# Optimization experiments

Measured on AMD Instinct MI355X. Metric: run time of the kernel, lower is better.

Reference implementation:

```python
import jax, jax.numpy as jnp
import numpy as np

B, L, V = 64, 512, 32000
E, H, D = 64, 512, 1024   # embed dim, LSTM hidden, bidirectional dim
NH, KD = 8, 64            # attention heads, key_dim
TOPK = 5
BN_EPS = 1e-3             # keras BatchNormalization default epsilon


def _run_lstm(x, Wx, Wh, b):
    """Keras-style LSTM (gate order i,f,g,o). x: [B,T,Din]. Returns (seq [B,T,H], last [B,H])."""
    Bn, Hn = x.shape[0], Wh.shape[0]
    z = jnp.einsum('btd,dk->btk', x, Wx) + b  # precompute input contribution [B,T,4H]
    def step(carry, zt):
        h, c = carry
        g = zt + h @ Wh
        i, f, gg, o = jnp.split(g, 4, axis=-1)
        c = jax.nn.sigmoid(f) * c + jax.nn.sigmoid(i) * jnp.tanh(gg)
        h = jax.nn.sigmoid(o) * jnp.tanh(c)
        return (h, c), h
    init = (jnp.zeros((Bn, Hn), x.dtype), jnp.zeros((Bn, Hn), x.dtype))
    (hT, _), hs = jax.lax.scan(step, init, jnp.swapaxes(z, 0, 1))
    return jnp.swapaxes(hs, 0, 1), hT


def _bilstm_seq(x, fWx, fWh, fb, bWx, bWh, bb):
    hf, _ = _run_lstm(x, fWx, fWh, fb)
    hb, _ = _run_lstm(x[:, ::-1], bWx, bWh, bb)
    return jnp.concatenate([hf, hb[:, ::-1]], axis=-1)


def _bilstm_last(x, fWx, fWh, fb, bWx, bWh, bb):
    _, hf = _run_lstm(x, fWx, fWh, fb)
    _, hb = _run_lstm(x[:, ::-1], bWx, bWh, bb)
    return jnp.concatenate([hf, hb], axis=-1)


def _cos(x):
    return x / (jnp.linalg.norm(x, axis=-1, keepdims=True) + 1e-6)


def _topk_gather(q, keys, values, k, weight=None):
    """Cosine-similarity top-k retrieval: q [B,64], keys/values [N,64] -> [B,k,64]."""
    sim = _cos(q) @ _cos(keys).T          # [B,N]
    if weight is not None:
        sim = sim * weight                # importance / confidence weighting
    _, idx = jax.lax.top_k(sim, k)
    return values[idx]                    # gather -> [B,k,64]


def _forward(tokens, emb,
             l1f_Wx, l1f_Wh, l1f_b, l1b_Wx, l1b_Wh, l1b_b,
             l2f_Wx, l2f_Wh, l2f_b, l2b_Wx, l2b_Wh, l2b_b,
             Wq, bq, Wk, bk, Wv, bv, Wo, bo,
             mq_W, mq_b,
             ext_keys, ext_vals, form_emb, conc_keys, conc_vals,
             st_mem, lt_mem, lt_imp, inf_mem, inf_conf,
             rs_W, rs_b, bn_gamma, bn_beta, bn_mean, bn_var,
             out_W, out_b, fin_W, fin_b):
    # _process_input
    x = emb[tokens]                                                   # [B,L,64]
    x = _bilstm_seq(x, l1f_Wx, l1f_Wh, l1f_b, l1b_Wx, l1b_Wh, l1b_b)  # [B,L,1024]
    x = _bilstm_last(x, l2f_Wx, l2f_Wh, l2f_b, l2b_Wx, l2b_Wh, l2b_b) # [B,1024]
    # _apply_attention: MHA over a length-1 sequence
    xs = x[:, None, :]                                                # [B,1,1024]
    q = jnp.einsum('bse,ehd->bshd', xs, Wq) + bq
    k = jnp.einsum('bse,ehd->bshd', xs, Wk) + bk
    v = jnp.einsum('bse,ehd->bshd', xs, Wv) + bv
    att = jax.nn.softmax(jnp.einsum('bshd,bthd->bhst', q, k) / jnp.sqrt(jnp.float32(KD)), axis=-1)
    ctx = jnp.einsum('bhst,bthd->bshd', att, v)
    x = (jnp.einsum('bshd,hde->bse', ctx, Wo) + bo)[:, 0]             # [B,1024]
    # _query_memories: six-bank gather/combine
    query = x @ mq_W + mq_b                                           # [B,64]
    m_ext = jax.nn.softmax(query @ ext_keys.T, axis=-1) @ ext_vals    # [B,64]
    m_form = _topk_gather(query, form_emb, form_emb, TOPK)            # [B,5,64]
    m_conc = _topk_gather(query, conc_keys, conc_vals, TOPK)          # [B,5,64]
    m_st = _topk_gather(query, st_mem, st_mem, TOPK)                  # [B,5,64]
    m_lt = _topk_gather(query, lt_mem, lt_mem, TOPK, weight=lt_imp)   # [B,5,64]
    m_inf = _topk_gather(query, inf_mem, inf_mem, TOPK, weight=inf_conf)
    mem = jnp.concatenate([m_ext[:, None], m_form, m_conc, m_st, m_lt, m_inf], axis=1)  # [B,26,64]
    x = jnp.mean(mem, axis=1)                                         # [B,64]
    # _apply_reasoning (training=False -> inference batchnorm)
    x = jax.nn.relu(x @ rs_W + rs_b)                                  # [B,512]
    x = (x - bn_mean) / jnp.sqrt(bn_var + BN_EPS) * bn_gamma + bn_beta
    # _generate_output (stage 'elementary1')
    x = x @ out_W + out_b                                             # [B,128]
    return jax.nn.sigmoid(x @ fin_W + fin_b)                          # [B,1]


def setup_inputs() -> dict:
    key = jax.random.key(0)
    ks = iter(jax.random.split(key, 64))
    def rn(shape, s=0.02):
        return jax.random.normal(next(ks), shape, dtype=jnp.float32) * s
    def z(shape):
        return jnp.zeros(shape, dtype=jnp.float32)
    inp = {
        'tokens': jax.random.randint(next(ks), (B, L), 0, V),
        'emb': rn((V, E), 0.05),
        'l1f_Wx': rn((E, 4 * H)), 'l1f_Wh': rn((H, 4 * H)), 'l1f_b': z((4 * H,)),
        'l1b_Wx': rn((E, 4 * H)), 'l1b_Wh': rn((H, 4 * H)), 'l1b_b': z((4 * H,)),
        'l2f_Wx': rn((D, 4 * H)), 'l2f_Wh': rn((H, 4 * H)), 'l2f_b': z((4 * H,)),
        'l2b_Wx': rn((D, 4 * H)), 'l2b_Wh': rn((H, 4 * H)), 'l2b_b': z((4 * H,)),
        'Wq': rn((D, NH, KD)), 'bq': z((NH, KD)),
        'Wk': rn((D, NH, KD)), 'bk': z((NH, KD)),
        'Wv': rn((D, NH, KD)), 'bv': z((NH, KD)),
        'Wo': rn((NH, KD, D)), 'bo': z((D,)),
        'mq_W': rn((D, 64)), 'mq_b': z((64,)),
        'ext_keys': rn((100, 64), 0.5), 'ext_vals': rn((100, 64), 0.5),
        'form_emb': rn((1000, 64), 0.5),
        'conc_keys': rn((1000, 64), 0.5), 'conc_vals': rn((1000, 64), 0.5),
        'st_mem': rn((100, 64), 0.5),
        'lt_mem': rn((10000, 64), 0.5),
        'lt_imp': jax.random.uniform(next(ks), (10000,), dtype=jnp.float32),
        'inf_mem': rn((500, 64), 0.5),
        'inf_conf': jax.random.uniform(next(ks), (500,), dtype=jnp.float32),
        'rs_W': rn((64, 512)), 'rs_b': z((512,)),
        'bn_gamma': jnp.ones((512,), jnp.float32), 'bn_beta': z((512,)),
        'bn_mean': rn((512,), 0.1), 'bn_var': jnp.ones((512,), jnp.float32),
        'out_W': rn((512, 128)), 'out_b': z((128,)),
        'fin_W': rn((128, 1)), 'fin_b': z((1,)),
    }
    return inp


def reference(tokens, emb,
              l1f_Wx, l1f_Wh, l1f_b, l1b_Wx, l1b_Wh, l1b_b,
              l2f_Wx, l2f_Wh, l2f_b, l2b_Wx, l2b_Wh, l2b_b,
              Wq, bq, Wk, bk, Wv, bv, Wo, bo,
              mq_W, mq_b,
              ext_keys, ext_vals, form_emb, conc_keys, conc_vals,
              st_mem, lt_mem, lt_imp, inf_mem, inf_conf,
              rs_W, rs_b, bn_gamma, bn_beta, bn_mean, bn_var,
              out_W, out_b, fin_W, fin_b):
    return _forward(tokens, emb,
                    l1f_Wx, l1f_Wh, l1f_b, l1b_Wx, l1b_Wh, l1b_b,
                    l2f_Wx, l2f_Wh, l2f_b, l2b_Wx, l2b_Wh, l2b_b,
                    Wq, bq, Wk, bk, Wv, bv, Wo, bo,
                    mq_W, mq_b,
                    ext_keys, ext_vals, form_emb, conc_keys, conc_vals,
                    st_mem, lt_mem, lt_imp, inf_mem, inf_conf,
                    rs_W, rs_b, bn_gamma, bn_beta, bn_mean, bn_var,
                    out_W, out_b, fin_W, fin_b)
```

## Files before the change

kernel.cpp:

```cpp
#include <hip/hip_runtime.h>
#include <cstddef>
#include <cstdint>

typedef short s8v   __attribute__((ext_vector_type(8)));
typedef float f32x4 __attribute__((ext_vector_type(4)));

__device__ __forceinline__ float b2f(unsigned short u) {
  union { unsigned u; float f; } x; x.u = ((unsigned)u) << 16; return x.f;
}
__device__ __forceinline__ unsigned short f2b(float f) {
  union { float f; unsigned u; } x; x.f = f;
  unsigned u = x.u;
  return (unsigned short)((u + 0x7FFFu + ((u >> 16) & 1u)) >> 16);
}
__device__ __forceinline__ float sigm(float x) { return 1.f / (1.f + __expf(-x)); }
__device__ __forceinline__ float tanh_(float x) { return 1.f - 2.f / (__expf(2.f * x) + 1.f); }

#define AT_LOAD(p)        __hip_atomic_load((p), __ATOMIC_RELAXED, __HIP_MEMORY_SCOPE_AGENT)
#define AT_STORE_RLX(p,v) __hip_atomic_store((p), (v), __ATOMIC_RELAXED, __HIP_MEMORY_SCOPE_AGENT)

__device__ __forceinline__ s8v ldg_b128_sc(const unsigned short* p) {
  s8v r;
  asm volatile("global_load_dwordx4 %0, %1, off sc0 sc1" : "=v"(r) : "v"(p) : "memory");
  return r;
}
__device__ __forceinline__ void stg_b128_sc(unsigned short* p, s8v v) {
  asm volatile("global_store_dwordx4 %0, %1, off sc0 sc1" :: "v"(p), "v"(v) : "memory");
}

__global__ void __launch_bounds__(256)
k_embed(const int* __restrict__ tok, const float* __restrict__ emb,
        unsigned short* __restrict__ x1t)
{
  const int g = blockIdx.x * 256 + threadIdx.x;
  if (g >= 64 * 512 * 8) return;
  const int row = g >> 3, i = g & 7;
  const int b = row >> 9, t = row & 511;
  const int tk = tok[row];
  const f32x4 v0 = *(const f32x4*)(emb + (size_t)tk * 64 + i * 8);
  const f32x4 v1 = *(const f32x4*)(emb + (size_t)tk * 64 + i * 8 + 4);
  s8v o;
#pragma unroll
  for (int e = 0; e < 4; ++e) { o[e] = (short)f2b(v0[e]); o[4 + e] = (short)f2b(v1[e]); }
  *(s8v*)(x1t + ((size_t)t * 64 + b) * 64 + i * 8) = o;
}

__global__ void __launch_bounds__(256)
k_tr(const float* __restrict__ Wf, const float* __restrict__ Wb,
     unsigned short* __restrict__ out, int K, int N)
{
  __shared__ float t[64][65];
  const int tid = threadIdx.x;
  const int kt = blockIdx.x, nt = blockIdx.y, dir = blockIdx.z;
  const float* W = dir ? Wb : Wf;
#pragma unroll
  for (int i = 0; i < 16; ++i) {
    const int c = i * 256 + tid;
    const int k = c >> 6, n = c & 63;
    t[k][n] = W[(size_t)(kt * 64 + k) * N + nt * 64 + n];
  }
  __syncthreads();
#pragma unroll
  for (int i = 0; i < 16; ++i) {
    const int c = i * 256 + tid;
    const int n = c >> 6, k = c & 63;
    out[(size_t)dir * N * K + (size_t)(nt * 64 + n) * K + kt * 64 + k] = f2b(t[k][n]);
  }
}

__global__ void __launch_bounds__(256)
k_norms(const float* __restrict__ formE, const float* __restrict__ concK,
        const float* __restrict__ stM, const float* __restrict__ ltM,
        const float* __restrict__ infM, float* __restrict__ inn)
{
  const int i = blockIdx.x * 256 + threadIdx.x;
  if (i >= 12600) return;
  const float* src; int loc;
  if (i < 1000)       { src = formE; loc = i; }
  else if (i < 2000)  { src = concK; loc = i - 1000; }
  else if (i < 2100)  { src = stM;   loc = i - 2000; }
  else if (i < 12100) { src = ltM;   loc = i - 2100; }
  else                { src = infM;  loc = i - 12100; }
  float ss = 0.f;
#pragma unroll 16
  for (int d = 0; d < 64; ++d) { const float v = src[(size_t)loc * 64 + d]; ss += v * v; }
  inn[i] = 1.f / (sqrtf(ss) + 1e-6f);
}

template<int PHASE>
__global__ void __launch_bounds__(128, 1)
k_lstm(const unsigned short* __restrict__ x1t,
       const unsigned short* __restrict__ z2fp, const unsigned short* __restrict__ z2bp,
       const unsigned short* __restrict__ wht,
       const float* __restrict__ Wxf, const float* __restrict__ Wxb,
       const float* __restrict__ bsf, const float* __restrict__ bsb,
       unsigned short* __restrict__ hbuf,
       unsigned short* __restrict__ yout,
       int* __restrict__ flags,
       float* __restrict__ cg,
       int s0, int s1, int CT)
{
  __shared__ __align__(16) unsigned short wh_lds[64 * 512];
  __shared__ __align__(16) unsigned short z_lds[64 * 72];
  __shared__ __align__(16) unsigned short hout[16 * 72];

  const int tid  = threadIdx.x;
  const int w    = tid >> 6;
  const int lane = tid & 63;
  const int fc   = lane & 15, fg = lane >> 4;
  const int wg   = blockIdx.x & 31;
  const int dir  = blockIdx.x >> 5;
  const int j0   = wg * 16;

  const unsigned short* Wht = wht + (size_t)dir * 2048 * 512;
  const float* Wx = dir ? Wxb : Wxf;
  const unsigned short* Z2 = dir ? z2bp : z2fp;
  const float* BS = dir ? bsb : bsf;
  int* flg = flags + dir * 64;
  unsigned short* hb = hbuf + (size_t)dir * (2 * 64 * 512);

  float bias_reg[4];
#pragma unroll
  for (int nt = 0; nt < 4; ++nt) bias_reg[nt] = BS[nt * 512 + j0 + fc];

  float c_reg[8];
  if (PHASE == 1 || s0 == 0) {
#pragma unroll
    for (int i = 0; i < 8; ++i) c_reg[i] = 0.f;
  } else {
#pragma unroll
    for (int mt = 0; mt < 2; ++mt)
#pragma unroll
      for (int v = 0; v < 4; ++v)
        c_reg[mt * 4 + v] =
          cg[(size_t)dir * 32768 + (size_t)(w * 32 + mt * 16 + fg * 4 + v) * 512 + j0 + fc];
  }

#pragma unroll
  for (int i = 0; i < 32; ++i) {
    const int c = i * 128 + tid;
    const int lc = c >> 6, kq8 = c & 63;
    const int nt = lc >> 4, fcc = lc & 15;
    s8v v = *(const s8v*)(Wht + (size_t)(nt * 512 + j0 + fcc) * 512 + kq8 * 8);
    *(s8v*)((char*)wh_lds + lc * 1024 + ((kq8 * 16) ^ ((lc & 7) << 4))) = v;
  }

  s8v Bx[4][2];
  if (PHASE == 1) {
#pragma unroll
    for (int nt = 0; nt < 4; ++nt)
#pragma unroll
      for (int kx = 0; kx < 2; ++kx) {
        s8v f;
#pragma unroll
        for (int i = 0; i < 8; ++i)
          f[i] = (short)f2b(Wx[(size_t)(kx * 32 + fg * 8 + i) * 2048 + nt * 512 + j0 + fc]);
        Bx[nt][kx] = f;
      }
  }
  __syncthreads();

  for (int s = s0; s < s1; ++s) {
    const int t = dir ? (511 - s) : s;
    const int gb = tid >> 1, jh = tid & 1;

    s8v xf[2][2];
    if (PHASE == 1) {
#pragma unroll
      for (int mt = 0; mt < 2; ++mt)
#pragma unroll
        for (int kx = 0; kx < 2; ++kx)
          xf[mt][kx] = *(const s8v*)(x1t +
            ((size_t)t * 64 + (w * 32 + mt * 16 + fc)) * 64 + kx * 32 + fg * 8);
    } else {
      const int lt = dir ? (s1 - 1 - s) : (s - s0);
      s8v zr[4];
#pragma unroll
      for (int g = 0; g < 4; ++g)
        zr[g] = *(const s8v*)(Z2 + ((size_t)(gb * CT + lt)) * 2048 + g * 512 + j0 + jh * 8);
#pragma unroll
      for (int g = 0; g < 4; ++g)
        *(s8v*)(z_lds + gb * 72 + g * 16 + jh * 8) = zr[g];
    }

    f32x4 acc[2][4];
#pragma unroll
    for (int mt = 0; mt < 2; ++mt)
#pragma unroll
      for (int nt = 0; nt < 4; ++nt) acc[mt][nt] = (f32x4){0.f, 0.f, 0.f, 0.f};

    if (s > 0) {
      const int target = s;
      int spins = 0;
      for (;;) {
        int v = AT_LOAD(&flg[lane]);
        if (__all(v >= target)) break;
        if (++spins > (1 << 18)) break;
        __builtin_amdgcn_s_sleep(1);
      }
    }

    if (PHASE == 1) {
#pragma unroll
      for (int kx = 0; kx < 2; ++kx)
#pragma unroll
        for (int mt = 0; mt < 2; ++mt)
#pragma unroll
          for (int nt = 0; nt < 4; ++nt)
            acc[mt][nt] = __builtin_amdgcn_mfma_f32_16x16x32_bf16(xf[mt][kx], Bx[nt][kx], acc[mt][nt], 0, 0, 0);
    }

    if (s > 0) {
      const unsigned short* hsrc = hb + (size_t)((s - 1) & 1) * (64 * 512);
      s8v af[32];
#pragma unroll
      for (int kk = 0; kk < 16; ++kk)
#pragma unroll
        for (int mt = 0; mt < 2; ++mt)
          af[kk * 2 + mt] = ldg_b128_sc(hsrc +
            (size_t)((kk * 4 + fg) * 64 + (w * 32 + mt * 16 + fc)) * 8);

      asm volatile("s_waitcnt vmcnt(16)" ::: "memory");
      __builtin_amdgcn_sched_barrier(0);
#pragma unroll
      for (int kk = 0; kk < 8; ++kk) {
        const int k2 = (kk * 32 + fg * 8) * 2;
        s8v bh[4];
#pragma unroll
        for (int nt = 0; nt < 4; ++nt) {
          const int lc = nt * 16 + fc;
          bh[nt] = *(const s8v*)((char*)wh_lds + lc * 1024 + (k2 ^ ((lc & 7) << 4)));
        }
#pragma unroll
        for (int mt = 0; mt < 2; ++mt)
#pragma unroll
          for (int nt = 0; nt < 4; ++nt)
            acc[mt][nt] = __builtin_amdgcn_mfma_f32_16x16x32_bf16(af[kk * 2 + mt], bh[nt], acc[mt][nt], 0, 0, 0);
      }
      asm volatile("s_waitcnt vmcnt(0)" ::: "memory");
      __builtin_amdgcn_sched_barrier(0);
#pragma unroll
      for (int kk = 8; kk < 16; ++kk) {
        const int k2 = (kk * 32 + fg * 8) * 2;
        s8v bh[4];
#pragma unroll
        for (int nt = 0; nt < 4; ++nt) {
          const int lc = nt * 16 + fc;
          bh[nt] = *(const s8v*)((char*)wh_lds + lc * 1024 + (k2 ^ ((lc & 7) << 4)));
        }
#pragma unroll
        for (int mt = 0; mt < 2; ++mt)
#pragma unroll
          for (int nt = 0; nt < 4; ++nt)
            acc[mt][nt] = __builtin_amdgcn_mfma_f32_16x16x32_bf16(af[kk * 2 + mt], bh[nt], acc[mt][nt], 0, 0, 0);
      }
    }

    if (PHASE == 2) {
      asm volatile("s_waitcnt lgkmcnt(0)" ::: "memory");
      __builtin_amdgcn_sched_barrier(0);
    }
#pragma unroll
    for (int mt = 0; mt < 2; ++mt)
#pragma unroll
      for (int v = 0; v < 4; ++v) {
        const int b = w * 32 + mt * 16 + fg * 4 + v;
        float pi = acc[mt][0][v] + bias_reg[0];
        float pf = acc[mt][1][v] + bias_reg[1];
        float pg = acc[mt][2][v] + bias_reg[2];
        float po = acc[mt][3][v] + bias_reg[3];
        if (PHASE == 2) {
          pi += b2f(z_lds[b * 72 + 0 * 16 + fc]);
          pf += b2f(z_lds[b * 72 + 1 * 16 + fc]);
          pg += b2f(z_lds[b * 72 + 2 * 16 + fc]);
          po += b2f(z_lds[b * 72 + 3 * 16 + fc]);
        }
        const float c = sigm(pf) * c_reg[mt * 4 + v] + sigm(pi) * tanh_(pg);
        c_reg[mt * 4 + v] = c;
        hout[fc * 72 + b] = f2b(sigm(po) * tanh_(c));
      }
    asm volatile("s_waitcnt lgkmcnt(0)" ::: "memory");
    __builtin_amdgcn_sched_barrier(0);
    {
      const int bb = tid >> 1, hh = tid & 1;
      s8v o;
#pragma unroll
      for (int e = 0; e < 8; ++e) o[e] = (short)hout[(hh * 8 + e) * 72 + bb];
      stg_b128_sc(hb + (size_t)(s & 1) * (64 * 512) +
                  (size_t)(((j0 >> 3) + hh) * 64 + bb) * 8, o);
      if (PHASE == 1) {
        *(s8v*)(yout + ((size_t)(bb * 512 + t)) * 1024 + dir * 512 + j0 + hh * 8) = o;
      } else if (s == 511) {
        *(s8v*)(yout + (size_t)bb * 1024 + dir * 512 + j0 + hh * 8) = o;
      }
    }
    if (PHASE == 2 && s == s1 - 1 && s1 < 512) {
#pragma unroll
      for (int mt = 0; mt < 2; ++mt)
#pragma unroll
        for (int v = 0; v < 4; ++v)
          cg[(size_t)dir * 32768 + (size_t)(w * 32 + mt * 16 + fg * 4 + v) * 512 + j0 + fc] =
            c_reg[mt * 4 + v];
    }
    asm volatile("s_waitcnt vmcnt(0)" ::: "memory");
    __builtin_amdgcn_sched_barrier(0);
    if (lane == 0) AT_STORE_RLX(&flg[wg * 2 + w], s + 1);
  }
}

__global__ void __launch_bounds__(256)
k_zgemm(const unsigned short* __restrict__ A, const unsigned short* __restrict__ Wxt,
        unsigned short* __restrict__ Cf, unsigned short* __restrict__ Cb,
        int tb0, int tb1, int CT)
{
  __shared__ unsigned short As[128 * 64];
  __shared__ unsigned short Bs[128 * 64];
  const int tid = threadIdx.x;
  const int lane = tid & 63;
  const int w = tid >> 6;
  const int wm = w >> 1, wn = w & 1;
  const int bx = blockIdx.x, by = blockIdx.y, dz = blockIdx.z;
  const unsigned short* Bmat = Wxt + (size_t)dz * 2048 * 1024;
  unsigned short* C = dz ? Cb : Cf;
  const int tb = dz ? tb1 : tb0;
  const int fc = lane & 15, fk = (lane >> 4) << 3;

  f32x4 acc[4][4];
#pragma unroll
  for (int mt = 0; mt < 4; ++mt)
#pragma unroll
    for (int nt = 0; nt < 4; ++nt) acc[mt][nt] = (f32x4){0.f, 0.f, 0.f, 0.f};

  for (int kt = 0; kt < 16; ++kt) {
    __syncthreads();
#pragma unroll
    for (int i = 0; i < 4; ++i) {
      const int c = i * 256 + tid;
      const int row = c >> 3, kb = c & 7;
      const int m = by * 128 + row;
      const int b = m / CT, lt = m - b * CT;
      s8v v = *(const s8v*)(A + ((size_t)b * 512 + tb + lt) * 1024 + kt * 64 + kb * 8);
      *(s8v*)((char*)As + row * 128 + ((kb * 16) ^ ((row & 7) << 4))) = v;
    }
#pragma unroll
    for (int i = 0; i < 4; ++i) {
      const int c = i * 256 + tid;
      const int n = c >> 3, kb = c & 7;
      s8v v = *(const s8v*)(Bmat + (size_t)(bx * 128 + n) * 1024 + kt * 64 + kb * 8);
      *(s8v*)((char*)Bs + n * 128 + ((kb * 16) ^ ((n & 7) << 4))) = v;
    }
    __syncthreads();
#pragma unroll
    for (int kk = 0; kk < 2; ++kk) {
      const int k2 = (kk * 32 + fk) * 2;
      s8v a[4], bfr[4];
#pragma unroll
      for (int mt = 0; mt < 4; ++mt) {
        const int row = wm * 64 + mt * 16 + fc;
        a[mt] = *(const s8v*)((char*)As + row * 128 + (k2 ^ ((row & 7) << 4)));
      }
#pragma unroll
      for (int nt = 0; nt < 4; ++nt) {
        const int n = wn * 64 + nt * 16 + fc;
        bfr[nt] = *(const s8v*)((char*)Bs + n * 128 + (k2 ^ ((n & 7) << 4)));
      }
#pragma unroll
      for (int mt = 0; mt < 4; ++mt)
#pragma unroll
        for (int nt = 0; nt < 4; ++nt)
          acc[mt][nt] = __builtin_amdgcn_mfma_f32_16x16x32_bf16(a[mt], bfr[nt], acc[mt][nt], 0, 0, 0);
    }
  }
  const int r0 = (lane >> 4) << 2;
#pragma unroll
  for (int mt = 0; mt < 4; ++mt)
#pragma unroll
    for (int nt = 0; nt < 4; ++nt) {
      const size_t rowg = (size_t)(by * 128 + wm * 64 + mt * 16 + r0);
      const int colg = bx * 128 + wn * 64 + nt * 16 + fc;
#pragma unroll
      for (int r = 0; r < 4; ++r)
        C[(rowg + r) * 2048 + colg] = f2b(acc[mt][nt][r]);
    }
}

__global__ void __launch_bounds__(256)
k_head1(const unsigned short* __restrict__ x2,
        const float* __restrict__ Wv, const float* __restrict__ bv,
        const float* __restrict__ Wo, const float* __restrict__ bo,
        const float* __restrict__ mqW, const float* __restrict__ mqb,
        float* __restrict__ query)
{
  __shared__ float xs[1024], ys[512], x3[1024];
  __shared__ float part[4][64];
  const int b = blockIdx.x, tid = threadIdx.x;
  for (int i = tid; i < 1024; i += 256) xs[i] = b2f(x2[(size_t)b * 1024 + i]);
  __syncthreads();
  {
    const int o = tid * 2;
    float a0 = 0.f, a1 = 0.f;
#pragma unroll 8
    for (int e = 0; e < 1024; ++e) {
      const float xv = xs[e];
      a0 += xv * Wv[(size_t)e * 512 + o];
      a1 += xv * Wv[(size_t)e * 512 + o + 1];
    }
    ys[o] = a0 + bv[o];
    ys[o + 1] = a1 + bv[o + 1];
  }
  __syncthreads();
  {
    const int e0 = tid * 4;
    float a0 = 0.f, a1 = 0.f, a2 = 0.f, a3 = 0.f;
#pragma unroll 8
    for (int h = 0; h < 512; ++h) {
      const float yv = ys[h];
      a0 += yv * Wo[(size_t)h * 1024 + e0];
      a1 += yv * Wo[(size_t)h * 1024 + e0 + 1];
      a2 += yv * Wo[(size_t)h * 1024 + e0 + 2];
      a3 += yv * Wo[(size_t)h * 1024 + e0 + 3];
    }
    x3[e0] = a0 + bo[e0];
    x3[e0 + 1] = a1 + bo[e0 + 1];
    x3[e0 + 2] = a2 + bo[e0 + 2];
    x3[e0 + 3] = a3 + bo[e0 + 3];
  }
  __syncthreads();
  {
    const int o = tid & 63, kc = tid >> 6;
    float a = 0.f;
#pragma unroll 8
    for (int e = kc * 256; e < kc * 256 + 256; ++e) a += x3[e] * mqW[(size_t)e * 64 + o];
    part[kc][o] = a;
  }
  __syncthreads();
  if (tid < 64)
    query[b * 64 + tid] = part[0][tid] + part[1][tid] + part[2][tid] + part[3][tid] + mqb[tid];
}

__device__ void bank_topk(const float* __restrict__ K, const float* __restrict__ V,
                          int n, const float* __restrict__ W, const float* __restrict__ inn,
                          float qinv, const float* q, float* sims, float* red, int* redi,
                          float* acc64, int tid)
{
  for (int i = tid; i < n; i += 256) {
    float s = 0.f;
#pragma unroll 16
    for (int d = 0; d < 64; ++d) s += q[d] * K[(size_t)i * 64 + d];
    s *= qinv * inn[i];
    if (W) s *= W[i];
    sims[i] = s;
  }
  __syncthreads();
  for (int it = 0; it < 5; ++it) {
    float bv = -1e30f; int bi = 1 << 30;
    for (int i = tid; i < n; i += 256) {
      const float v = sims[i];
      if (v > bv) { bv = v; bi = i; }
    }
    red[tid] = bv; redi[tid] = bi;
    __syncthreads();
    for (int st = 128; st >= 1; st >>= 1) {
      if (tid < st) {
        const float v = red[tid + st]; const int ix = redi[tid + st];
        if (v > red[tid] || (v == red[tid] && ix < redi[tid])) { red[tid] = v; redi[tid] = ix; }
      }
      __syncthreads();
    }
    const int sel = redi[0];
    if (tid < 64) acc64[tid] += V[(size_t)sel * 64 + tid];
    if (tid == 0) sims[sel] = -1e30f;
    __syncthreads();
  }
}

__global__ void __launch_bounds__(256)
k_head2(const float* __restrict__ query,
        const float* extK, const float* extV,
        const float* formE, const float* concK, const float* concV,
        const float* stM, const float* ltM, const float* ltW,
        const float* infM, const float* infW,
        const float* __restrict__ inn,
        const float* rsW, const float* rsb,
        const float* gma, const float* bta,
        const float* mea, const float* vr,
        const float* outW, const float* outb,
        const float* finW, const float* finb,
        float* __restrict__ out)
{
  __shared__ float q[64];
  __shared__ float acc64[64];
  __shared__ float sims[10000];
  __shared__ float red[256];
  __shared__ int redi[256];
  __shared__ float r1[512];
  __shared__ float o2[128];

  const int b = blockIdx.x, tid = threadIdx.x;
  if (tid < 64) q[tid] = query[b * 64 + tid];
  __syncthreads();
  red[tid] = (tid < 64) ? q[tid] * q[tid] : 0.f;
  __syncthreads();
  for (int st = 128; st >= 1; st >>= 1) { if (tid < st) red[tid] += red[tid + st]; __syncthreads(); }
  const float qinv = 1.f / (sqrtf(red[0]) + 1e-6f);
  __syncthreads();

  if (tid < 100) {
    float s = 0.f;
#pragma unroll 16
    for (int d = 0; d < 64; ++d) s += q[d] * extK[(size_t)tid * 64 + d];
    sims[tid] = s;
  }
  __syncthreads();
  red[tid] = (tid < 100) ? sims[tid] : -1e30f;
  __syncthreads();
  for (int st = 128; st >= 1; st >>= 1) { if (tid < st && red[tid + st] > red[tid]) red[tid] = red[tid + st]; __syncthreads(); }
  const float mx = red[0];
  __syncthreads();
  red[tid] = (tid < 100) ? __expf(sims[tid] - mx) : 0.f;
  __syncthreads();
  for (int st = 128; st >= 1; st >>= 1) { if (tid < st) red[tid] += red[tid + st]; __syncthreads(); }
  const float Z = red[0];
  __syncthreads();
  if (tid < 100) sims[tid] = __expf(sims[tid] - mx) / Z;
  __syncthreads();
  if (tid < 64) {
    float a = 0.f;
    for (int i = 0; i < 100; ++i) a += sims[i] * extV[(size_t)i * 64 + tid];
    acc64[tid] = a;
  }
  __syncthreads();

  bank_topk(formE, formE, 1000,  nullptr, inn + 0,     qinv, q, sims, red, redi, acc64, tid);
  bank_topk(concK, concV, 1000,  nullptr, inn + 1000,  qinv, q, sims, red, redi, acc64, tid);
  bank_topk(stM,   stM,   100,   nullptr, inn + 2000,  qinv, q, sims, red, redi, acc64, tid);
  bank_topk(ltM,   ltM,   10000, ltW,     inn + 2100,  qinv, q, sims, red, redi, acc64, tid);
  bank_topk(infM,  infM,  500,   infW,    inn + 12100, qinv, q, sims, red, redi, acc64, tid);

  if (tid < 64) acc64[tid] *= (1.f / 26.f);
  __syncthreads();

  {
    const int o = tid * 2;
    float a0 = 0.f, a1 = 0.f;
#pragma unroll 16
    for (int d = 0; d < 64; ++d) {
      const float xv = acc64[d];
      a0 += xv * rsW[(size_t)d * 512 + o];
      a1 += xv * rsW[(size_t)d * 512 + o + 1];
    }
    a0 = fmaxf(a0 + rsb[o], 0.f);
    a1 = fmaxf(a1 + rsb[o + 1], 0.f);
    r1[o]     = (a0 - mea[o])     / sqrtf(vr[o]     + 1e-3f) * gma[o]     + bta[o];
    r1[o + 1] = (a1 - mea[o + 1]) / sqrtf(vr[o + 1] + 1e-3f) * gma[o + 1] + bta[o + 1];
  }
  __syncthreads();
  if (tid < 128) {
    float a = 0.f;
#pragma unroll 8
    for (int j = 0; j < 512; ++j) a += r1[j] * outW[(size_t)j * 128 + tid];
    o2[tid] = a + outb[tid];
  }
  __syncthreads();
  red[tid] = (tid < 128) ? o2[tid] * finW[tid] : 0.f;
  __syncthreads();
  for (int st = 128; st >= 1; st >>= 1) { if (tid < st) red[tid] += red[tid + st]; __syncthreads(); }
  if (tid == 0) out[b] = sigm(red[0] + finb[0]);
}

__global__ void k_diag(float* out, int n, float val) {
  const int i = blockIdx.x * 64 + threadIdx.x;
  if (i < n) out[i] = val;
}

extern "C" void kernel_launch(void* const* d_in, const int* in_sizes, int n_in,
                              void* d_out, int out_size, void* d_ws, size_t ws_size,
                              hipStream_t stream)
{
  (void)in_sizes; (void)n_in;
  const int*   tokens = (const int*)d_in[0];
  const float* emb    = (const float*)d_in[1];
  const float* l1fWx  = (const float*)d_in[2];
  const float* l1fWh  = (const float*)d_in[3];
  const float* l1fb   = (const float*)d_in[4];
  const float* l1bWx  = (const float*)d_in[5];
  const float* l1bWh  = (const float*)d_in[6];
  const float* l1bb   = (const float*)d_in[7];
  const float* l2fWx  = (const float*)d_in[8];
  const float* l2fWh  = (const float*)d_in[9];
  const float* l2fb   = (const float*)d_in[10];
  const float* l2bWx  = (const float*)d_in[11];
  const float* l2bWh  = (const float*)d_in[12];
  const float* l2bb   = (const float*)d_in[13];
  const float* Wv     = (const float*)d_in[18];
  const float* bv     = (const float*)d_in[19];
  const float* Wo     = (const float*)d_in[20];
  const float* bo     = (const float*)d_in[21];
  const float* mqW    = (const float*)d_in[22];
  const float* mqb    = (const float*)d_in[23];
  const float* extK   = (const float*)d_in[24];
  const float* extV   = (const float*)d_in[25];
  const float* formE  = (const float*)d_in[26];
  const float* concK  = (const float*)d_in[27];
  const float* concV  = (const float*)d_in[28];
  const float* stM    = (const float*)d_in[29];
  const float* ltM    = (const float*)d_in[30];
  const float* ltW    = (const float*)d_in[31];
  const float* infM   = (const float*)d_in[32];
  const float* infW   = (const float*)d_in[33];
  const float* rsW    = (const float*)d_in[34];
  const float* rsb    = (const float*)d_in[35];
  const float* gma    = (const float*)d_in[36];
  const float* bta    = (const float*)d_in[37];
  const float* mea    = (const float*)d_in[38];
  const float* vr     = (const float*)d_in[39];
  const float* outW   = (const float*)d_in[40];
  const float* outb   = (const float*)d_in[41];
  const float* finW   = (const float*)d_in[42];
  const float* finb   = (const float*)d_in[43];

  float* outp = (float*)d_out;
  char* ws = (char*)d_ws;

  size_t off = 0;
  auto take = [&](size_t sz) { size_t o = off; off += (sz + 255) & ~(size_t)255; return o; };
  const size_t o_x1    = take((size_t)64 * 512 * 64 * 2);
  const size_t o_y1    = take((size_t)64 * 512 * 1024 * 2);
  const size_t o_wxt   = take((size_t)2 * 2048 * 1024 * 2);
  const size_t o_wht1  = take((size_t)2 * 2048 * 512 * 2);
  const size_t o_wht2  = take((size_t)2 * 2048 * 512 * 2);
  const size_t o_h1    = take((size_t)2 * 2 * 64 * 512 * 2);
  const size_t o_h2    = take((size_t)2 * 2 * 64 * 512 * 2);
  const size_t o_cg    = take((size_t)2 * 64 * 512 * 4);
  const size_t o_x2    = take((size_t)64 * 1024 * 2);
  const size_t o_query = take((size_t)64 * 64 * 4);
  const size_t o_norms = take((size_t)12600 * 4);
  const size_t o_flags = take(1024);
  const size_t base = off;

  int CT = 0;
  const int cts[6] = {512, 256, 128, 64, 32, 16};
  for (int i = 0; i < 6; ++i) {
    const size_t need = base + (size_t)cts[i] * 524288 + 256;
    if (need <= ws_size) { CT = cts[i]; break; }
  }
  if (CT == 0) {
    k_diag<<<1, 64, 0, stream>>>(outp, out_size, (float)(ws_size >> 20));
    return;
  }
  const size_t o_zc = take((size_t)CT * 524288);

  unsigned short* x1t  = (unsigned short*)(ws + o_x1);
  unsigned short* y1   = (unsigned short*)(ws + o_y1);
  unsigned short* wxt  = (unsigned short*)(ws + o_wxt);
  unsigned short* wht1 = (unsigned short*)(ws + o_wht1);
  unsigned short* wht2 = (unsigned short*)(ws + o_wht2);
  unsigned short* h1   = (unsigned short*)(ws + o_h1);
  unsigned short* h2   = (unsigned short*)(ws + o_h2);
  float*          cg   = (float*)(ws + o_cg);
  unsigned short* x2   = (unsigned short*)(ws + o_x2);
  float*          qry  = (float*)(ws + o_query);
  float*          nrm  = (float*)(ws + o_norms);
  int*            flags = (int*)(ws + o_flags);
  unsigned short* zcf  = (unsigned short*)(ws + o_zc);
  unsigned short* zcb  = zcf + (size_t)64 * CT * 2048;

  hipMemsetAsync(flags, 0, 1024, stream);
  k_embed<<<1024, 256, 0, stream>>>(tokens, emb, x1t);
  k_norms<<<50, 256, 0, stream>>>(formE, concK, stM, ltM, infM, nrm);
  k_tr<<<dim3(8, 32, 2), 256, 0, stream>>>(l1fWh, l1bWh, wht1, 512, 2048);
  k_tr<<<dim3(8, 32, 2), 256, 0, stream>>>(l2fWh, l2bWh, wht2, 512, 2048);
  k_tr<<<dim3(16, 32, 2), 256, 0, stream>>>(l2fWx, l2bWx, wxt, 1024, 2048);

  k_lstm<1><<<64, 128, 0, stream>>>(x1t, nullptr, nullptr, wht1, l1fWx, l1bWx,
                                    l1fb, l1bb, h1, y1, flags, nullptr, 0, 512, 512);

  const int nC = 512 / CT;
  for (int c = 0; c < nC; ++c) {
    const int s0 = c * CT, s1 = s0 + CT;
    k_zgemm<<<dim3(16, (64 * CT) / 128, 2), 256, 0, stream>>>(
        y1, wxt, zcf, zcb, s0, 512 - s1, CT);
    k_lstm<2><<<64, 128, 0, stream>>>(nullptr, zcf, zcb, wht2, nullptr, nullptr,
                                      l2fb, l2bb, h2, x2, flags + 128, cg, s0, s1, CT);
  }

  k_head1<<<64, 256, 0, stream>>>(x2, Wv, bv, Wo, bo, mqW, mqb, qry);
  k_head2<<<64, 256, 0, stream>>>(qry, extK, extV, formE, concK, concV, stM, ltM, ltW,
                                  infM, infW, nrm, rsW, rsb, gma, bta, mea, vr,
                                  outW, outb, finW, finb, outp);
}
```

Before: 5.974 ms.

## Replace LSTM flag barrier with step-tagged hidden-state polling

Removes the per-step atomic flag array and spin-wait used to synchronize the persistent LSTM blocks. Each writer now encodes two bits of the step index in the low mantissa bits of the first two bf16 values of each 16-byte hidden-state store. Readers repeatedly reload only the chunks whose tags do not match yet, so the data load itself serves as the synchronization. This cuts a flag round-trip and store fence from every timestep, but slightly perturbs the hidden state values. It also gives up the split load/compute overlap, and correctness relies on 16-byte stores being seen atomically.

Result: slower. 6.424 ms (+7.5%).

```diff
diff --git a/kernel.cpp b/kernel.cpp
--- a/kernel.cpp
+++ b/kernel.cpp
@@ -15,9 +15,6 @@
 }
 __device__ __forceinline__ float sigm(float x) { return 1.f / (1.f + __expf(-x)); }
 __device__ __forceinline__ float tanh_(float x) { return 1.f - 2.f / (__expf(2.f * x) + 1.f); }
-
-#define AT_LOAD(p)        __hip_atomic_load((p), __ATOMIC_RELAXED, __HIP_MEMORY_SCOPE_AGENT)
-#define AT_STORE_RLX(p,v) __hip_atomic_store((p), (v), __ATOMIC_RELAXED, __HIP_MEMORY_SCOPE_AGENT)
 
 __device__ __forceinline__ s8v ldg_b128_sc(const unsigned short* p) {
   s8v r;
@@ -96,7 +93,6 @@
        const float* __restrict__ bsf, const float* __restrict__ bsb,
        unsigned short* __restrict__ hbuf,
        unsigned short* __restrict__ yout,
-       int* __restrict__ flags,
        float* __restrict__ cg,
        int s0, int s1, int CT)
 {
@@ -116,7 +112,6 @@
   const float* Wx = dir ? Wxb : Wxf;
   const unsigned short* Z2 = dir ? z2bp : z2fp;
   const float* BS = dir ? bsb : bsf;
-  int* flg = flags + dir * 64;
   unsigned short* hb = hbuf + (size_t)dir * (2 * 64 * 512);
 
   float bias_reg[4];
@@ -189,17 +184,6 @@
 #pragma unroll
       for (int nt = 0; nt < 4; ++nt) acc[mt][nt] = (f32x4){0.f, 0.f, 0.f, 0.f};
 
-    if (s > 0) {
-      const int target = s;
-      int spins = 0;
-      for (;;) {
-        int v = AT_LOAD(&flg[lane]);
-        if (__all(v >= target)) break;
-        if (++spins > (1 << 18)) break;
-        __builtin_amdgcn_s_sleep(1);
-      }
-    }
-
     if (PHASE == 1) {
 #pragma unroll
       for (int kx = 0; kx < 2; ++kx)
@@ -212,35 +196,38 @@
 
     if (s > 0) {
       const unsigned short* hsrc = hb + (size_t)((s - 1) & 1) * (64 * 512);
+      const short tb0 = (short)((s - 1) & 1);
+      const short tb1 = (short)(((s - 1) >> 1) & 1);
       s8v af[32];
-#pragma unroll
-      for (int kk = 0; kk < 16; ++kk)
-#pragma unroll
-        for (int mt = 0; mt < 2; ++mt)
-          af[kk * 2 + mt] = ldg_b128_sc(hsrc +
-            (size_t)((kk * 4 + fg) * 64 + (w * 32 + mt * 16 + fc)) * 8);
-
-      asm volatile("s_waitcnt vmcnt(16)" ::: "memory");
+      unsigned pend = 0xFFFFFFFFu;
+      int tries = 0;
+      for (;;) {
+#pragma unroll
+        for (int i = 0; i < 32; ++i) {
+          if (pend & (1u << i)) {
+            const int kk = i >> 1, mt = i & 1;
+            af[i] = ldg_b128_sc(hsrc +
+              (size_t)((kk * 4 + fg) * 64 + (w * 32 + mt * 16 + fc)) * 8);
+          }
+        }
+        asm volatile("s_waitcnt vmcnt(0)" ::: "memory");
+        __builtin_amdgcn_sched_barrier(0);
+        unsigned np = 0;
+#pragma unroll
+        for (int i = 0; i < 32; ++i) {
+          if (pend & (1u << i)) {
+            if (((af[i][0] & 1) != tb0) | ((af[i][1] & 1) != tb1)) np |= (1u << i);
+          }
+        }
+        pend = np;
+        if (!__any(pend != 0)) break;
+        if (++tries > (1 << 14)) break;
+        __builtin_amdgcn_s_sleep(1);
+      }
       __builtin_amdgcn_sched_barrier(0);
-#pragma unroll
-      for (int kk = 0; kk < 8; ++kk) {
-        const int k2 = (kk * 32 + fg * 8) * 2;
-        s8v bh[4];
-#pragma unroll
-        for (int nt = 0; nt < 4; ++nt) {
-          const int lc = nt * 16 + fc;
-          bh[nt] = *(const s8v*)((char*)wh_lds + lc * 1024 + (k2 ^ ((lc & 7) << 4)));
-        }
-#pragma unroll
-        for (int mt = 0; mt < 2; ++mt)
-#pragma unroll
-          for (int nt = 0; nt < 4; ++nt)
-            acc[mt][nt] = __builtin_amdgcn_mfma_f32_16x16x32_bf16(af[kk * 2 + mt], bh[nt], acc[mt][nt], 0, 0, 0);
-      }
-      asm volatile("s_waitcnt vmcnt(0)" ::: "memory");
-      __builtin_amdgcn_sched_barrier(0);
-#pragma unroll
-      for (int kk = 8; kk < 16; ++kk) {
+
+#pragma unroll
+      for (int kk = 0; kk < 16; ++kk) {
         const int k2 = (kk * 32 + fg * 8) * 2;
         s8v bh[4];
 #pragma unroll
@@ -286,8 +273,11 @@
       s8v o;
 #pragma unroll
       for (int e = 0; e < 8; ++e) o[e] = (short)hout[(hh * 8 + e) * 72 + bb];
+      s8v ot = o;
+      ot[0] = (short)((ot[0] & ~1) | (short)(s & 1));
+      ot[1] = (short)((ot[1] & ~1) | (short)((s >> 1) & 1));
       stg_b128_sc(hb + (size_t)(s & 1) * (64 * 512) +
-                  (size_t)(((j0 >> 3) + hh) * 64 + bb) * 8, o);
+                  (size_t)(((j0 >> 3) + hh) * 64 + bb) * 8, ot);
       if (PHASE == 1) {
         *(s8v*)(yout + ((size_t)(bb * 512 + t)) * 1024 + dir * 512 + j0 + hh * 8) = o;
       } else if (s == 511) {
@@ -302,9 +292,6 @@
           cg[(size_t)dir * 32768 + (size_t)(w * 32 + mt * 16 + fg * 4 + v) * 512 + j0 + fc] =
             c_reg[mt * 4 + v];
     }
-    asm volatile("s_waitcnt vmcnt(0)" ::: "memory");
-    __builtin_amdgcn_sched_barrier(0);
-    if (lane == 0) AT_STORE_RLX(&flg[wg * 2 + w], s + 1);
   }
 }
 
@@ -635,7 +622,6 @@
   const size_t o_x2    = take((size_t)64 * 1024 * 2);
   const size_t o_query = take((size_t)64 * 64 * 4);
   const size_t o_norms = take((size_t)12600 * 4);
-  const size_t o_flags = take(1024);
   const size_t base = off;
 
   int CT = 0;
@@ -661,11 +647,9 @@
   unsigned short* x2   = (unsigned short*)(ws + o_x2);
   float*          qry  = (float*)(ws + o_query);
   float*          nrm  = (float*)(ws + o_norms);
-  int*            flags = (int*)(ws + o_flags);
   unsigned short* zcf  = (unsigned short*)(ws + o_zc);
   unsigned short* zcb  = zcf + (size_t)64 * CT * 2048;
 
-  hipMemsetAsync(flags, 0, 1024, stream);
   k_embed<<<1024, 256, 0, stream>>>(tokens, emb, x1t);
   k_norms<<<50, 256, 0, stream>>>(formE, concK, stM, ltM, infM, nrm);
   k_tr<<<dim3(8, 32, 2), 256, 0, stream>>>(l1fWh, l1bWh, wht1, 512, 2048);
@@ -673,7 +657,7 @@
   k_tr<<<dim3(16, 32, 2), 256, 0, stream>>>(l2fWx, l2bWx, wxt, 1024, 2048);
 
   k_lstm<1><<<64, 128, 0, stream>>>(x1t, nullptr, nullptr, wht1, l1fWx, l1bWx,
-                                    l1fb, l1bb, h1, y1, flags, nullptr, 0, 512, 512);
+                                    l1fb, l1bb, h1, y1, nullptr, 0, 512, 512);
 
   const int nC = 512 / CT;
   for (int c = 0; c < nC; ++c) {
@@ -681,7 +665,7 @@
     k_zgemm<<<dim3(16, (64 * CT) / 128, 2), 256, 0, stream>>>(
         y1, wxt, zcf, zcb, s0, 512 - s1, CT);
     k_lstm<2><<<64, 128, 0, stream>>>(nullptr, zcf, zcb, wht2, nullptr, nullptr,
-                                      l2fb, l2bb, h2, x2, flags + 128, cg, s0, s1, CT);
+                                      l2fb, l2bb, h2, x2, cg, s0, s1, CT);
   }
 
   k_head1<<<64, 256, 0, stream>>>(x2, Wv, bv, Wo, bo, mqW, mqb, qry);
```
